# Performance work log

Hardware: AMD Instinct MI355X
Metric: run time of the kernel (lower is better)

## Reference

```python
import jax, jax.numpy as jnp
import numpy as np

BLKQ = 64
BLKK = 64
TOPK_RATIO = 0.125  # ratio of key blocks kept per query block


def setup_inputs() -> dict:
    key = jax.random.key(0)
    k0, k1, k2, k3 = jax.random.split(key, 4)
    B, H, L, D = 2, 16, 2048, 128
    q = jax.random.normal(k0, (B, H, L, D), dtype=jnp.float32)
    k = jax.random.normal(k1, (B, H, L, D), dtype=jnp.float32)
    v = jax.random.normal(k2, (B, H, L, D), dtype=jnp.float32)
    # proj_l is zero-init in the module; use small random weights so the branch is exercised
    w_proj = jax.random.normal(k3, (D, D), dtype=jnp.float32) * 0.02
    b_proj = jnp.zeros((D,), dtype=jnp.float32)
    return {"q": q, "k": k, "v": v, "w_proj": w_proj, "b_proj": b_proj}


def _forward(q, k, v, w_proj, b_proj):
    B, H, L, D = q.shape
    nQ, nK = L // BLKQ, L // BLKK
    real_topk = max(1, int(TOPK_RATIO * nK))
    scale = 1.0 / jnp.sqrt(jnp.float32(D))

    # ---- block map (get_block_map): mean-pooled block scores -> top-k key blocks per query block ----
    qb = q.reshape(B, H, nQ, BLKQ, D).mean(axis=3)            # (B,H,nQ,D)
    kb = k.reshape(B, H, nK, BLKK, D).mean(axis=3)            # (B,H,nK,D)
    blk_scores = jnp.einsum('bhqd,bhkd->bhqk', qb, kb)        # (B,H,nQ,nK)
    _, lut = jax.lax.top_k(jax.lax.stop_gradient(blk_scores), real_topk)  # (B,H,nQ,T) int32

    # ---- block-sparse softmax attention over the selected key blocks ----
    kblk = k.reshape(B, H, nK, BLKK, D)
    vblk = v.reshape(B, H, nK, BLKK, D)
    idx = lut[:, :, :, :, None, None]                         # (B,H,nQ,T,1,1)
    kg = jnp.take_along_axis(kblk[:, :, None], idx, axis=3)   # (B,H,nQ,T,BLKK,D)
    vg = jnp.take_along_axis(vblk[:, :, None], idx, axis=3)   # (B,H,nQ,T,BLKK,D)
    T = real_topk
    kg = kg.reshape(B, H, nQ, T * BLKK, D)
    vg = vg.reshape(B, H, nQ, T * BLKK, D)
    qr = q.reshape(B, H, nQ, BLKQ, D)
    s = jnp.einsum('bhqid,bhqjd->bhqij', qr, kg) * scale      # (B,H,nQ,BLKQ,T*BLKK)
    p = jax.nn.softmax(s, axis=-1)
    o_s = jnp.einsum('bhqij,bhqjd->bhqid', p, vg).reshape(B, H, L, D)

    # ---- linear (kernelized) attention branch, feature_map = softmax over D ----
    phi_q = jax.nn.softmax(q, axis=-1)
    phi_k = jax.nn.softmax(k, axis=-1)
    kvsum = jnp.einsum('bhld,bhle->bhde', phi_k, v)           # (B,H,D,D)
    ksum = phi_k.sum(axis=2)                                  # (B,H,D)
    num = jnp.einsum('bhld,bhde->bhle', phi_q, kvsum)         # (B,H,L,D)
    den = 1e-5 + jnp.einsum('bhld,bhd->bhl', phi_q, ksum)[..., None]
    o_l = num / den
    o_l = o_l @ w_proj.T + b_proj                             # nn.Linear

    return o_s + o_l                                          # (B,H,L,D)


def reference(q, k, v, w_proj, b_proj):
    return _forward(q, k, v, w_proj, b_proj)
```

## Files before the change

### kernel.cpp

```cpp
#include <hip/hip_runtime.h>
#include <math.h>

static constexpr int BH   = 32;
static constexpr int L    = 2048;
static constexpr int D    = 128;
static constexpr int NB   = 32;
static constexpr int TOPK = 4;

static constexpr size_t QB_OFF    = 0;
static constexpr size_t KB_OFF    = 131072;
static constexpr size_t LUT_OFF   = 262144;
static constexpr size_t KS_OFF    = 266240;
static constexpr size_t A_OFF     = 270336;
static constexpr size_t PART_OFF  = 794624;
static constexpr size_t KHI_OFF   = 9183232;
static constexpr size_t KLO_OFF   = 13377536;
static constexpr size_t VTHI_OFF  = 17571840;
static constexpr size_t VTLO_OFF  = 21766144;
static constexpr size_t PHITH_OFF = 25960448;
static constexpr size_t PHITL_OFF = 30154752;

typedef __attribute__((ext_vector_type(8))) short short8;
typedef __attribute__((ext_vector_type(4))) float f32x4;

__device__ __forceinline__ unsigned short f2bf(float x) {
  unsigned u = __float_as_uint(x);
  u += 0x7fffu + ((u >> 16) & 1u);
  return (unsigned short)(u >> 16);
}
__device__ __forceinline__ float bf2f(unsigned short h) {
  return __uint_as_float(((unsigned)h) << 16);
}
__device__ __forceinline__ f32x4 mfma16(short8 a, short8 b, f32x4 c) {
  return __builtin_amdgcn_mfma_f32_16x16x32_bf16(a, b, c, 0, 0, 0);
}
__device__ __forceinline__ void gl_lds16(const void* g, void* l) {
  __builtin_amdgcn_global_load_lds(
      (const __attribute__((address_space(1))) unsigned int*)g,
      (__attribute__((address_space(3))) unsigned int*)l, 16, 0, 0);
}

__global__ __launch_bounds__(256) void k_prep(
    const float* __restrict__ q, const float* __restrict__ k, const float* __restrict__ v,
    float* __restrict__ qb, float* __restrict__ kb,
    unsigned short* __restrict__ khi, unsigned short* __restrict__ klo,
    unsigned short* __restrict__ vthi, unsigned short* __restrict__ vtlo,
    unsigned short* __restrict__ phith, unsigned short* __restrict__ phitl,
    float* __restrict__ ksum) {
  extern __shared__ float smp[];
  float* Vs   = smp;
  float* Ps   = smp + 8192;
  float* part = smp + 16384;
  int bid = blockIdx.x;
  int t = threadIdx.x;
  size_t rb = (size_t)bid * 64 * D;
  int c = t & 31, g = t >> 5;
  const float4* v4 = (const float4*)(v + rb);
  float4* Vs4 = (float4*)Vs;
  float4* Ps4 = (float4*)Ps;
#pragma unroll
  for (int it = 0; it < 8; ++it) {
    int p = t + 256 * it;
    int row = p >> 5, cq = p & 31;
    Vs4[row * 32 + (cq ^ ((row >> 2) & 7))] = v4[p];
  }
  float4 qs = {0.f, 0.f, 0.f, 0.f};
#pragma unroll
  for (int it = 0; it < 8; ++it) {
    int row = g + 8 * it;
    float4 xv = *(const float4*)(q + rb + (size_t)row * D + 4 * c);
    qs.x += xv.x; qs.y += xv.y; qs.z += xv.z; qs.w += xv.w;
  }
  ((float4*)part)[g * 32 + c] = qs;
  __syncthreads();
  if (t < 128) {
    float s = 0.f;
#pragma unroll
    for (int gg = 0; gg < 8; ++gg) s += part[gg * 128 + t];
    qb[(size_t)bid * D + t] = s * (1.f / 64.f);
  }
  __syncthreads();
  float4 ks = {0.f, 0.f, 0.f, 0.f};
#pragma unroll
  for (int it = 0; it < 8; ++it) {
    int row = g + 8 * it;
    size_t off = rb + (size_t)row * D + 4 * c;
    float4 xv = *(const float4*)(k + off);
    ushort4 h, l;
    h.x = f2bf(xv.x); l.x = f2bf(xv.x - bf2f(h.x));
    h.y = f2bf(xv.y); l.y = f2bf(xv.y - bf2f(h.y));
    h.z = f2bf(xv.z); l.z = f2bf(xv.z - bf2f(h.z));
    h.w = f2bf(xv.w); l.w = f2bf(xv.w - bf2f(h.w));
    *(ushort4*)(khi + off) = h;
    *(ushort4*)(klo + off) = l;
    ks.x += xv.x; ks.y += xv.y; ks.z += xv.z; ks.w += xv.w;
    float mx = fmaxf(fmaxf(xv.x, xv.y), fmaxf(xv.z, xv.w));
    mx = fmaxf(mx, __shfl_xor(mx, 1));
    mx = fmaxf(mx, __shfl_xor(mx, 2));
    mx = fmaxf(mx, __shfl_xor(mx, 4));
    mx = fmaxf(mx, __shfl_xor(mx, 8));
    mx = fmaxf(mx, __shfl_xor(mx, 16));
    float e0 = __expf(xv.x - mx), e1 = __expf(xv.y - mx);
    float e2 = __expf(xv.z - mx), e3 = __expf(xv.w - mx);
    float es = e0 + e1 + e2 + e3;
    es += __shfl_xor(es, 1);
    es += __shfl_xor(es, 2);
    es += __shfl_xor(es, 4);
    es += __shfl_xor(es, 8);
    es += __shfl_xor(es, 16);
    float inv = 1.f / es;
    Ps4[row * 32 + (c ^ ((row >> 2) & 7))] =
        make_float4(e0 * inv, e1 * inv, e2 * inv, e3 * inv);
  }
  ((float4*)part)[g * 32 + c] = ks;
  __syncthreads();
  if (t < 128) {
    float s = 0.f;
#pragma unroll
    for (int gg = 0; gg < 8; ++gg) s += part[gg * 128 + t];
    kb[(size_t)bid * D + t] = s * (1.f / 64.f);
  }
  __syncthreads();
  size_t tb = (size_t)bid * 8192;
#pragma unroll
  for (int pp = 0; pp < 4; ++pp) {
    int d = 32 * pp + (t >> 3);
    int jc = t & 7;
    unsigned hs[8], ls[8], phs[8], pls[8];
#pragma unroll
    for (int i = 0; i < 8; ++i) {
      int j = jc * 8 + i;
      int idx = j * 128 + (d ^ (j & 28));
      float x = Vs[idx];
      unsigned short hh = f2bf(x);
      hs[i] = hh; ls[i] = f2bf(x - bf2f(hh));
      float px = Ps[idx];
      unsigned short phh = f2bf(px);
      phs[i] = phh; pls[i] = f2bf(px - bf2f(phh));
    }
    int4 hw, lw, pw, qw;
    hw.x = (int)(hs[0] | (hs[1] << 16)); hw.y = (int)(hs[2] | (hs[3] << 16));
    hw.z = (int)(hs[4] | (hs[5] << 16)); hw.w = (int)(hs[6] | (hs[7] << 16));
    lw.x = (int)(ls[0] | (ls[1] << 16)); lw.y = (int)(ls[2] | (ls[3] << 16));
    lw.z = (int)(ls[4] | (ls[5] << 16)); lw.w = (int)(ls[6] | (ls[7] << 16));
    pw.x = (int)(phs[0] | (phs[1] << 16)); pw.y = (int)(phs[2] | (phs[3] << 16));
    pw.z = (int)(phs[4] | (phs[5] << 16)); pw.w = (int)(phs[6] | (phs[7] << 16));
    qw.x = (int)(pls[0] | (pls[1] << 16)); qw.y = (int)(pls[2] | (pls[3] << 16));
    qw.z = (int)(pls[4] | (pls[5] << 16)); qw.w = (int)(pls[6] | (pls[7] << 16));
    *(int4*)(vthi  + tb + (size_t)d * 64 + jc * 8) = hw;
    *(int4*)(vtlo  + tb + (size_t)d * 64 + jc * 8) = lw;
    *(int4*)(phith + tb + (size_t)d * 64 + jc * 8) = pw;
    *(int4*)(phitl + tb + (size_t)d * 64 + jc * 8) = qw;
  }
  if (t < 128) {
    float s = 0.f;
#pragma unroll
    for (int row = 0; row < 64; ++row) s += Ps[row * 128 + (t ^ (row & 28))];
    atomicAdd(&ksum[(size_t)(bid >> 5) * D + t], s);
  }
}

__global__ __launch_bounds__(256) void k_scores_topk(
    const float* __restrict__ qb, const float* __restrict__ kb, int* __restrict__ lut) {
  __shared__ float qs[NB * D];
  __shared__ float ks[NB * 132];
  __shared__ float sc[NB * 33];
  int bh = blockIdx.x, t = threadIdx.x;
  const float4* qg = (const float4*)(qb + (size_t)bh * NB * D);
  const float4* kg = (const float4*)(kb + (size_t)bh * NB * D);
  float4* qs4 = (float4*)qs;
  float4* ks4 = (float4*)ks;
#pragma unroll
  for (int it = 0; it < 4; ++it) {
    int p = t + 256 * it;
    int row = p >> 5, c = p & 31;
    qs4[p] = qg[p];
    ks4[row * 33 + c] = kg[p];
  }
  __syncthreads();
#pragma unroll
  for (int ss = 0; ss < 4; ++ss) {
    int idx = t + 256 * ss;
    int qr = idx >> 5, kc = idx & 31;
    float acc = 0.f;
#pragma unroll
    for (int c = 0; c < 32; ++c) {
      float4 a = qs4[qr * 32 + c];
      float4 b = ks4[kc * 33 + c];
      acc += a.x * b.x + a.y * b.y + a.z * b.z + a.w * b.w;
    }
    sc[qr * 33 + kc] = acc;
  }
  __syncthreads();
  if (t < NB) {
    unsigned mask = 0;
    for (int s = 0; s < TOPK; ++s) {
      float best = -INFINITY; int bi = 0;
      for (int j = 0; j < NB; ++j) {
        float vv = sc[t * 33 + j];
        if (!((mask >> j) & 1u) && vv > best) { best = vv; bi = j; }
      }
      mask |= 1u << bi;
      lut[((size_t)(bh * NB) + t) * TOPK + s] = bi;
    }
  }
}

__global__ __launch_bounds__(256) void k_attn(
    const float* __restrict__ q,
    const unsigned short* __restrict__ khi, const unsigned short* __restrict__ klo,
    const unsigned short* __restrict__ vthi, const unsigned short* __restrict__ vtlo,
    const int* __restrict__ lut, float* __restrict__ out) {
  extern __shared__ char sm[];
  char* KsH = sm;
  char* KsL = sm + 16384;
  char* VsH = sm + 32768;
  char* VsL = sm + 49152;
  int f = blockIdx.x;
  int n = ((f & 7) << 7) | (f >> 3);
  int qblk = n & 31, bh = n >> 5;
  int t = threadIdx.x, lane = t & 63, w = t >> 6;
  char* PwH = sm + 65536 + w * 4096;
  char* PwL = PwH + 2048;
  int lr = lane & 15, lg = lane >> 4;
  const float scale = 0.088388347648318447f;

  short8 qh[4], ql[4];
  const float* qrow = q + ((size_t)bh * L + (size_t)qblk * 64 + 16 * w + lr) * D;
#pragma unroll
  for (int s = 0; s < 4; ++s) {
    float4 x0 = *(const float4*)(qrow + 32 * s + 8 * lg);
    float4 x1 = *(const float4*)(qrow + 32 * s + 8 * lg + 4);
    float xs[8] = {x0.x, x0.y, x0.z, x0.w, x1.x, x1.y, x1.z, x1.w};
    short8 hv, lv;
#pragma unroll
    for (int i = 0; i < 8; ++i) {
      unsigned short h = f2bf(xs[i]);
      hv[i] = (short)h;
      lv[i] = (short)f2bf(xs[i] - bf2f(h));
    }
    qh[s] = hv; ql[s] = lv;
  }

  f32x4 oacc[8];
#pragma unroll
  for (int i = 0; i < 8; ++i) oacc[i] = (f32x4){0.f, 0.f, 0.f, 0.f};
  float mrun = -INFINITY, lrun = 0.f;

  const int* lp = lut + ((size_t)bh * NB + qblk) * TOPK;
  for (int itb = 0; itb < TOPK; ++itb) {
    int kblk = lp[itb];
    __syncthreads();
    {
      const char* kbh = (const char*)(khi + ((size_t)bh * L + (size_t)kblk * 64) * D);
      const char* kbl = (const char*)(klo + ((size_t)bh * L + (size_t)kblk * 64) * D);
      const char* vbh = (const char*)(vthi + ((size_t)(bh * NB + kblk)) * 8192);
      const char* vbl = (const char*)(vtlo + ((size_t)(bh * NB + kblk)) * 8192);
#pragma unroll
      for (int jj = 0; jj < 4; ++jj) {
        int ib = 4 * w + jj;
        {
          int lrow = 4 * ib + (lane >> 4);
          int soff = lrow * 256 + (((lane & 15) ^ (lrow & 7)) << 4);
          gl_lds16(kbh + soff, KsH + ib * 1024);
          gl_lds16(kbl + soff, KsL + ib * 1024);
        }
        {
          int lrow = 8 * ib + (lane >> 3);
          int soff = lrow * 128 + (((lane & 7) ^ (lrow & 7)) << 4);
          gl_lds16(vbh + soff, VsH + ib * 1024);
          gl_lds16(vbl + soff, VsL + ib * 1024);
        }
      }
    }
    __syncthreads();
    f32x4 sacc[4];
#pragma unroll
    for (int i = 0; i < 4; ++i) sacc[i] = (f32x4){0.f, 0.f, 0.f, 0.f};
#pragma unroll
    for (int s = 0; s < 4; ++s) {
#pragma unroll
      for (int tk = 0; tk < 4; ++tk) {
        int krow = 16 * tk + lr;
        int off = krow * 256 + (((4 * s + lg) ^ (krow & 7)) << 4);
        short8 kH = *(const short8*)(KsH + off);
        short8 kL = *(const short8*)(KsL + off);
        sacc[tk] = mfma16(kH, qh[s], sacc[tk]);
        sacc[tk] = mfma16(kL, qh[s], sacc[tk]);
        sacc[tk] = mfma16(kH, ql[s], sacc[tk]);
      }
    }
    float mloc = -INFINITY;
#pragma unroll
    for (int tk = 0; tk < 4; ++tk)
#pragma unroll
      for (int r = 0; r < 4; ++r) mloc = fmaxf(mloc, sacc[tk][r]);
    mloc = fmaxf(mloc, __shfl_xor(mloc, 16));
    mloc = fmaxf(mloc, __shfl_xor(mloc, 32));
    float mnew = fmaxf(mrun, mloc * scale);
    float alpha = __expf(mrun - mnew);
    float lloc = 0.f;
#pragma unroll
    for (int tk = 0; tk < 4; ++tk) {
      unsigned ph[4], pl[4];
#pragma unroll
      for (int r = 0; r < 4; ++r) {
        float pf = __expf(sacc[tk][r] * scale - mnew);
        lloc += pf;
        unsigned short hh = f2bf(pf);
        ph[r] = hh; pl[r] = f2bf(pf - bf2f(hh));
      }
      int j0b = 32 * tk + 8 * lg;
      int slot16 = j0b >> 4, half = (j0b >> 3) & 1;
      int off = lr * 128 + ((slot16 ^ (lr & 7)) << 4) + half * 8;
      *(int2*)(PwH + off) = make_int2((int)(ph[0] | (ph[1] << 16)),
                                      (int)(ph[2] | (ph[3] << 16)));
      *(int2*)(PwL + off) = make_int2((int)(pl[0] | (pl[1] << 16)),
                                      (int)(pl[2] | (pl[3] << 16)));
    }
    lloc += __shfl_xor(lloc, 16);
    lloc += __shfl_xor(lloc, 32);
    lrun = lrun * alpha + lloc;
    mrun = mnew;
    float ar[4];
#pragma unroll
    for (int r = 0; r < 4; ++r) ar[r] = __shfl(alpha, 4 * lg + r);
#pragma unroll
    for (int tv = 0; tv < 8; ++tv)
#pragma unroll
      for (int r = 0; r < 4; ++r) oacc[tv][r] *= ar[r];
#pragma unroll
    for (int ks = 0; ks < 2; ++ks) {
      int poff = lr * 128 + (((lg + 4 * ks) ^ (lr & 7)) << 4);
      short8 pH = *(const short8*)(PwH + poff);
      short8 pL = *(const short8*)(PwL + poff);
#pragma unroll
      for (int tv = 0; tv < 8; ++tv) {
        int vrow = 16 * tv + lr;
        int voff = vrow * 128 + (((lg + 4 * ks) ^ (vrow & 7)) << 4);
        short8 vH = *(const short8*)(VsH + voff);
        short8 vL = *(const short8*)(VsL + voff);
        oacc[tv] = mfma16(pH, vH, oacc[tv]);
        oacc[tv] = mfma16(pL, vH, oacc[tv]);
        oacc[tv] = mfma16(pH, vL, oacc[tv]);
      }
    }
  }
  float rinv[4];
#pragma unroll
  for (int r = 0; r < 4; ++r) rinv[r] = 1.f / __shfl(lrun, 4 * lg + r);
  float* ob = out + ((size_t)bh * L + (size_t)qblk * 64 + 16 * w) * D;
#pragma unroll
  for (int tv = 0; tv < 8; ++tv)
#pragma unroll
    for (int r = 0; r < 4; ++r)
      ob[(size_t)(4 * lg + r) * D + 16 * tv + lr] = oacc[tv][r] * rinv[r];
}

__global__ __launch_bounds__(256) void k_kvmm(
    const unsigned short* __restrict__ vthi, const unsigned short* __restrict__ vtlo,
    const unsigned short* __restrict__ phith, const unsigned short* __restrict__ phitl,
    float* __restrict__ part) {
  int slice = blockIdx.x, bh = blockIdx.y;
  int t = threadIdx.x, lane = t & 63, w = t >> 6;
  int lr = lane & 15, lg = lane >> 4;
  f32x4 acc[2][8];
#pragma unroll
  for (int et = 0; et < 2; ++et)
#pragma unroll
    for (int dt = 0; dt < 8; ++dt) acc[et][dt] = (f32x4){0.f, 0.f, 0.f, 0.f};
#pragma unroll
  for (int ks = 0; ks < 4; ++ks) {
    int kblk = 2 * slice + (ks >> 1);
    int li = 32 * (ks & 1);
    size_t base = ((size_t)(bh * NB + kblk)) * 8192 + li + 8 * lg;
    short8 aH[2], aL[2];
#pragma unroll
    for (int et = 0; et < 2; ++et) {
      int e = 32 * w + 16 * et + lr;
      aH[et] = *(const short8*)(vthi + base + (size_t)e * 64);
      aL[et] = *(const short8*)(vtlo + base + (size_t)e * 64);
    }
#pragma unroll
    for (int dt = 0; dt < 8; ++dt) {
      int d = 16 * dt + lr;
      short8 bH = *(const short8*)(phith + base + (size_t)d * 64);
      short8 bL = *(const short8*)(phitl + base + (size_t)d * 64);
#pragma unroll
      for (int et = 0; et < 2; ++et) {
        acc[et][dt] = mfma16(aH[et], bH, acc[et][dt]);
        acc[et][dt] = mfma16(aL[et], bH, acc[et][dt]);
        acc[et][dt] = mfma16(aH[et], bL, acc[et][dt]);
      }
    }
  }
  float* pb = part + ((size_t)(bh * 16 + slice)) * 16384;
#pragma unroll
  for (int et = 0; et < 2; ++et)
#pragma unroll
    for (int dt = 0; dt < 8; ++dt)
#pragma unroll
      for (int r = 0; r < 4; ++r)
        pb[(size_t)(32 * w + 16 * et + 4 * lg + r) * 128 + 16 * dt + lr] =
            acc[et][dt][r];
}

__global__ __launch_bounds__(256) void k_projA(
    const float* __restrict__ part, const float* __restrict__ w, float* __restrict__ A) {
  extern __shared__ float smA[];
  float* wts   = smA;
  float* kvred = smA + 16384;
  int dquad = blockIdx.x, bh = blockIdx.y;
  int t = threadIdx.x;
  const float4* wg = (const float4*)w;
#pragma unroll
  for (int it = 0; it < 16; ++it) {
    int p4 = t + 256 * it;
    int j = p4 >> 5, ebase = (p4 & 31) << 2;
    float4 val = wg[p4];
    wts[(ebase + 0) * D + ((j + ebase + 0) & 127)] = val.x;
    wts[(ebase + 1) * D + ((j + ebase + 1) & 127)] = val.y;
    wts[(ebase + 2) * D + ((j + ebase + 2) & 127)] = val.z;
    wts[(ebase + 3) * D + ((j + ebase + 3) & 127)] = val.w;
  }
#pragma unroll
  for (int u = 0; u < 4; ++u) {
    int f4id = t + 256 * u;
    int e = f4id >> 3, dl4 = f4id & 7;
    float4 acc4 = {0.f, 0.f, 0.f, 0.f};
#pragma unroll
    for (int s = 0; s < 16; ++s) {
      float4 p = *(const float4*)(part + ((size_t)(bh * 16 + s)) * 16384 +
                                  (size_t)e * 128 + dquad * 32 + dl4 * 4);
      acc4.x += p.x; acc4.y += p.y; acc4.z += p.z; acc4.w += p.w;
    }
    *(float4*)(kvred + e * 32 + dl4 * 4) = acc4;
  }
  __syncthreads();
  int j = t & 127, dh = t >> 7;
  int dbase = dquad * 32 + dh * 16;
  float acc[16];
#pragma unroll
  for (int u = 0; u < 16; ++u) acc[u] = 0.f;
  for (int e = 0; e < D; ++e) {
    float wv = wts[e * D + ((j + e) & 127)];
#pragma unroll
    for (int dd = 0; dd < 16; ++dd)
      acc[dd] += kvred[e * 32 + dh * 16 + dd] * wv;
  }
#pragma unroll
  for (int dd = 0; dd < 16; ++dd)
    A[((size_t)(bh * D + dbase + dd)) * D + j] = acc[dd];
}

__global__ __launch_bounds__(256) void k_linear_out(
    const float* __restrict__ q, const float* __restrict__ A,
    const float* __restrict__ ksum, const float* __restrict__ bproj,
    float* __restrict__ out) {
  extern __shared__ float smf[];
  float* As    = smf;
  float* phis  = smf + 16384;
  float* ksums = smf + 16384 + 32 * 132;
  int rb = blockIdx.x, bh = blockIdx.y;
  int t = threadIdx.x;
  int r = t >> 3, sub = t & 7;
  const float4* Ag = (const float4*)(A + (size_t)bh * D * D);
  float4* As4 = (float4*)As;
#pragma unroll
  for (int it = 0; it < 16; ++it) {
    int p = t + 256 * it;
    As4[p] = Ag[p];
  }
  if (t < D) ksums[t] = ksum[bh * D + t];
  int row = rb * 32 + r;
  const float4* qr4 = (const float4*)(q + ((size_t)(bh * L + row)) * D) + sub * 4;
  float x[16];
  {
    float4 a0 = qr4[0], a1 = qr4[1], a2 = qr4[2], a3 = qr4[3];
    x[0]=a0.x; x[1]=a0.y; x[2]=a0.z; x[3]=a0.w;
    x[4]=a1.x; x[5]=a1.y; x[6]=a1.z; x[7]=a1.w;
    x[8]=a2.x; x[9]=a2.y; x[10]=a2.z; x[11]=a2.w;
    x[12]=a3.x; x[13]=a3.y; x[14]=a3.z; x[15]=a3.w;
  }
  float mx = -INFINITY;
#pragma unroll
  for (int u = 0; u < 16; ++u) mx = fmaxf(mx, x[u]);
  mx = fmaxf(mx, __shfl_xor(mx, 1));
  mx = fmaxf(mx, __shfl_xor(mx, 2));
  mx = fmaxf(mx, __shfl_xor(mx, 4));
  float es = 0.f;
#pragma unroll
  for (int u = 0; u < 16; ++u) { x[u] = __expf(x[u] - mx); es += x[u]; }
  es += __shfl_xor(es, 1);
  es += __shfl_xor(es, 2);
  es += __shfl_xor(es, 4);
  float inv = 1.f / es;
  __syncthreads();
  float dloc = 0.f;
#pragma unroll
  for (int u = 0; u < 16; ++u) {
    float ph = x[u] * inv;
    phis[r * 132 + sub * 16 + u] = ph;
    dloc += ph * ksums[sub * 16 + u];
  }
  dloc += __shfl_xor(dloc, 1);
  dloc += __shfl_xor(dloc, 2);
  dloc += __shfl_xor(dloc, 4);
  float rden = 1.f / (1e-5f + dloc);
  __syncthreads();
  float4 acc[4];
#pragma unroll
  for (int ee = 0; ee < 4; ++ee) { acc[ee].x = 0.f; acc[ee].y = 0.f; acc[ee].z = 0.f; acc[ee].w = 0.f; }
  for (int f = 0; f < D; ++f) {
    float ph = phis[r * 132 + f];
#pragma unroll
    for (int ee = 0; ee < 4; ++ee) {
      float4 av = As4[f * 32 + sub + (ee << 3)];
      acc[ee].x += ph * av.x;
      acc[ee].y += ph * av.y;
      acc[ee].z += ph * av.z;
      acc[ee].w += ph * av.w;
    }
  }
  float4* og = (float4*)(out + ((size_t)(bh * L + row)) * D);
  const float4* bg = (const float4*)bproj;
#pragma unroll
  for (int ee = 0; ee < 4; ++ee) {
    int c = sub + (ee << 3);
    float4 oo = og[c];
    float4 bb = bg[c];
    oo.x += acc[ee].x * rden + bb.x;
    oo.y += acc[ee].y * rden + bb.y;
    oo.z += acc[ee].z * rden + bb.z;
    oo.w += acc[ee].w * rden + bb.w;
    og[c] = oo;
  }
}

extern "C" void kernel_launch(void* const* d_in, const int* in_sizes, int n_in,
                              void* d_out, int out_size, void* d_ws, size_t ws_size,
                              hipStream_t stream) {
  const float* q = (const float*)d_in[0];
  const float* k = (const float*)d_in[1];
  const float* v = (const float*)d_in[2];
  const float* w = (const float*)d_in[3];
  const float* b = (const float*)d_in[4];
  float* out = (float*)d_out;
  float* ws = (float*)d_ws;
  float* qb    = ws + QB_OFF;
  float* kb    = ws + KB_OFF;
  int*   lut   = (int*)(ws + LUT_OFF);
  float* ksum  = ws + KS_OFF;
  float* A     = ws + A_OFF;
  float* partb = ws + PART_OFF;
  unsigned short* khi   = (unsigned short*)(ws + KHI_OFF);
  unsigned short* klo   = (unsigned short*)(ws + KLO_OFF);
  unsigned short* vthi  = (unsigned short*)(ws + VTHI_OFF);
  unsigned short* vtlo  = (unsigned short*)(ws + VTLO_OFF);
  unsigned short* phith = (unsigned short*)(ws + PHITH_OFF);
  unsigned short* phitl = (unsigned short*)(ws + PHITL_OFF);

  hipFuncSetAttribute(reinterpret_cast<const void*>(k_prep),
                      hipFuncAttributeMaxDynamicSharedMemorySize, 69632);
  hipFuncSetAttribute(reinterpret_cast<const void*>(k_attn),
                      hipFuncAttributeMaxDynamicSharedMemorySize, 81920);
  hipFuncSetAttribute(reinterpret_cast<const void*>(k_projA),
                      hipFuncAttributeMaxDynamicSharedMemorySize, 81920);
  hipFuncSetAttribute(reinterpret_cast<const void*>(k_linear_out),
                      hipFuncAttributeMaxDynamicSharedMemorySize, 82944);

  hipMemsetAsync(ksum, 0, 4096 * sizeof(float), stream);

  k_prep       <<<dim3(BH * NB), dim3(256), 69632, stream>>>(
      q, k, v, qb, kb, khi, klo, vthi, vtlo, phith, phitl, ksum);
  k_scores_topk<<<dim3(BH),      dim3(256), 0, stream>>>(qb, kb, lut);
  k_attn       <<<dim3(NB * BH), dim3(256), 81920, stream>>>(
      q, khi, klo, vthi, vtlo, lut, out);
  k_kvmm       <<<dim3(16, BH),  dim3(256), 0, stream>>>(
      vthi, vtlo, phith, phitl, partb);
  k_projA      <<<dim3(4, BH),   dim3(256), 81920, stream>>>(partb, w, A);
  k_linear_out <<<dim3(64, BH),  dim3(256), 82944, stream>>>(q, A, ksum, b, out);
}
```

Before: 331.2 us.

## Run linear-attention output GEMM on MFMA with split-bf16 transposed A

k_projA now writes the projected KV matrix transposed, as high and low bf16 halves. A new k_linout kernel replaces the scalar FP32 LDS-based k_linear_out: it computes phi(q) in registers, splits it into bf16 hi/lo, and runs the 64x128x128 product with three MFMA passes per tile, reading A directly from global memory. The aim is to replace scalar FMA work and the 80KB shared-memory staging with matrix cores and to use fewer, larger blocks. Precision relies on the three-term bf16 split, and A is now read from global or cache per wave.

```diff
diff --git a/kernel.cpp b/kernel.cpp
--- a/kernel.cpp
+++ b/kernel.cpp
@@ -11,7 +11,8 @@
 static constexpr size_t KB_OFF    = 131072;
 static constexpr size_t LUT_OFF   = 262144;
 static constexpr size_t KS_OFF    = 266240;
-static constexpr size_t A_OFF     = 270336;
+static constexpr size_t ATHI_OFF  = 270336;
+static constexpr size_t ATLO_OFF  = 532480;
 static constexpr size_t PART_OFF  = 794624;
 static constexpr size_t KHI_OFF   = 9183232;
 static constexpr size_t KLO_OFF   = 13377536;
@@ -406,7 +407,8 @@
 }
 
 __global__ __launch_bounds__(256) void k_projA(
-    const float* __restrict__ part, const float* __restrict__ w, float* __restrict__ A) {
+    const float* __restrict__ part, const float* __restrict__ w,
+    unsigned short* __restrict__ athi, unsigned short* __restrict__ atlo) {
   extern __shared__ float smA[];
   float* wts   = smA;
   float* kvred = smA + 16384;
@@ -448,92 +450,107 @@
     for (int dd = 0; dd < 16; ++dd)
       acc[dd] += kvred[e * 32 + dh * 16 + dd] * wv;
   }
-#pragma unroll
-  for (int dd = 0; dd < 16; ++dd)
-    A[((size_t)(bh * D + dbase + dd)) * D + j] = acc[dd];
-}
-
-__global__ __launch_bounds__(256) void k_linear_out(
-    const float* __restrict__ q, const float* __restrict__ A,
-    const float* __restrict__ ksum, const float* __restrict__ bproj,
-    float* __restrict__ out) {
-  extern __shared__ float smf[];
-  float* As    = smf;
-  float* phis  = smf + 16384;
-  float* ksums = smf + 16384 + 32 * 132;
-  int rb = blockIdx.x, bh = blockIdx.y;
-  int t = threadIdx.x;
-  int r = t >> 3, sub = t & 7;
-  const float4* Ag = (const float4*)(A + (size_t)bh * D * D);
-  float4* As4 = (float4*)As;
-#pragma unroll
-  for (int it = 0; it < 16; ++it) {
-    int p = t + 256 * it;
-    As4[p] = Ag[p];
-  }
-  if (t < D) ksums[t] = ksum[bh * D + t];
-  int row = rb * 32 + r;
-  const float4* qr4 = (const float4*)(q + ((size_t)(bh * L + row)) * D) + sub * 4;
-  float x[16];
-  {
-    float4 a0 = qr4[0], a1 = qr4[1], a2 = qr4[2], a3 = qr4[3];
-    x[0]=a0.x; x[1]=a0.y; x[2]=a0.z; x[3]=a0.w;
-    x[4]=a1.x; x[5]=a1.y; x[6]=a1.z; x[7]=a1.w;
-    x[8]=a2.x; x[9]=a2.y; x[10]=a2.z; x[11]=a2.w;
-    x[12]=a3.x; x[13]=a3.y; x[14]=a3.z; x[15]=a3.w;
-  }
+  unsigned hs[16], ls[16];
+#pragma unroll
+  for (int dd = 0; dd < 16; ++dd) {
+    unsigned short hh = f2bf(acc[dd]);
+    hs[dd] = hh; ls[dd] = f2bf(acc[dd] - bf2f(hh));
+  }
+  size_t ab = ((size_t)bh * D + j) * D + dbase;
+  int4 h0, h1, l0, l1;
+  h0.x = (int)(hs[0] | (hs[1] << 16));   h0.y = (int)(hs[2] | (hs[3] << 16));
+  h0.z = (int)(hs[4] | (hs[5] << 16));   h0.w = (int)(hs[6] | (hs[7] << 16));
+  h1.x = (int)(hs[8] | (hs[9] << 16));   h1.y = (int)(hs[10] | (hs[11] << 16));
+  h1.z = (int)(hs[12] | (hs[13] << 16)); h1.w = (int)(hs[14] | (hs[15] << 16));
+  l0.x = (int)(ls[0] | (ls[1] << 16));   l0.y = (int)(ls[2] | (ls[3] << 16));
+  l0.z = (int)(ls[4] | (ls[5] << 16));   l0.w = (int)(ls[6] | (ls[7] << 16));
+  l1.x = (int)(ls[8] | (ls[9] << 16));   l1.y = (int)(ls[10] | (ls[11] << 16));
+  l1.z = (int)(ls[12] | (ls[13] << 16)); l1.w = (int)(ls[14] | (ls[15] << 16));
+  *(int4*)(athi + ab) = h0;  *(int4*)(athi + ab + 8) = h1;
+  *(int4*)(atlo + ab) = l0;  *(int4*)(atlo + ab + 8) = l1;
+}
+
+__global__ __launch_bounds__(256) void k_linout(
+    const float* __restrict__ q, const unsigned short* __restrict__ athi,
+    const unsigned short* __restrict__ atlo, const float* __restrict__ ksum,
+    const float* __restrict__ bproj, float* __restrict__ out) {
+  int qblk = blockIdx.x, bh = blockIdx.y;
+  int t = threadIdx.x, lane = t & 63, w = t >> 6;
+  int lr = lane & 15, lg = lane >> 4;
+  const float* qrow = q + ((size_t)bh * L + (size_t)qblk * 64 + 16 * w + lr) * D;
+  float xs[4][8];
   float mx = -INFINITY;
 #pragma unroll
-  for (int u = 0; u < 16; ++u) mx = fmaxf(mx, x[u]);
-  mx = fmaxf(mx, __shfl_xor(mx, 1));
-  mx = fmaxf(mx, __shfl_xor(mx, 2));
-  mx = fmaxf(mx, __shfl_xor(mx, 4));
+  for (int s = 0; s < 4; ++s) {
+    float4 x0 = *(const float4*)(qrow + 32 * s + 8 * lg);
+    float4 x1 = *(const float4*)(qrow + 32 * s + 8 * lg + 4);
+    xs[s][0] = x0.x; xs[s][1] = x0.y; xs[s][2] = x0.z; xs[s][3] = x0.w;
+    xs[s][4] = x1.x; xs[s][5] = x1.y; xs[s][6] = x1.z; xs[s][7] = x1.w;
+#pragma unroll
+    for (int i = 0; i < 8; ++i) mx = fmaxf(mx, xs[s][i]);
+  }
+  mx = fmaxf(mx, __shfl_xor(mx, 16));
+  mx = fmaxf(mx, __shfl_xor(mx, 32));
   float es = 0.f;
 #pragma unroll
-  for (int u = 0; u < 16; ++u) { x[u] = __expf(x[u] - mx); es += x[u]; }
-  es += __shfl_xor(es, 1);
-  es += __shfl_xor(es, 2);
-  es += __shfl_xor(es, 4);
+  for (int s = 0; s < 4; ++s)
+#pragma unroll
+    for (int i = 0; i < 8; ++i) { xs[s][i] = __expf(xs[s][i] - mx); es += xs[s][i]; }
+  es += __shfl_xor(es, 16);
+  es += __shfl_xor(es, 32);
   float inv = 1.f / es;
-  __syncthreads();
-  float dloc = 0.f;
-#pragma unroll
-  for (int u = 0; u < 16; ++u) {
-    float ph = x[u] * inv;
-    phis[r * 132 + sub * 16 + u] = ph;
-    dloc += ph * ksums[sub * 16 + u];
-  }
-  dloc += __shfl_xor(dloc, 1);
-  dloc += __shfl_xor(dloc, 2);
-  dloc += __shfl_xor(dloc, 4);
-  float rden = 1.f / (1e-5f + dloc);
-  __syncthreads();
-  float4 acc[4];
-#pragma unroll
-  for (int ee = 0; ee < 4; ++ee) { acc[ee].x = 0.f; acc[ee].y = 0.f; acc[ee].z = 0.f; acc[ee].w = 0.f; }
-  for (int f = 0; f < D; ++f) {
-    float ph = phis[r * 132 + f];
-#pragma unroll
-    for (int ee = 0; ee < 4; ++ee) {
-      float4 av = As4[f * 32 + sub + (ee << 3)];
-      acc[ee].x += ph * av.x;
-      acc[ee].y += ph * av.y;
-      acc[ee].z += ph * av.z;
-      acc[ee].w += ph * av.w;
-    }
-  }
-  float4* og = (float4*)(out + ((size_t)(bh * L + row)) * D);
+  const float* kp = ksum + (size_t)bh * D;
+  float dpart = 0.f;
+  short8 phH[4], phL[4];
+#pragma unroll
+  for (int s = 0; s < 4; ++s) {
+    float4 k0 = *(const float4*)(kp + 32 * s + 8 * lg);
+    float4 k1 = *(const float4*)(kp + 32 * s + 8 * lg + 4);
+    float kk[8] = {k0.x, k0.y, k0.z, k0.w, k1.x, k1.y, k1.z, k1.w};
+    short8 hv, lv;
+#pragma unroll
+    for (int i = 0; i < 8; ++i) {
+      float p = xs[s][i] * inv;
+      dpart += p * kk[i];
+      unsigned short hh = f2bf(p);
+      hv[i] = (short)hh;
+      lv[i] = (short)f2bf(p - bf2f(hh));
+    }
+    phH[s] = hv; phL[s] = lv;
+  }
+  dpart += __shfl_xor(dpart, 16);
+  dpart += __shfl_xor(dpart, 32);
+  float rden = 1.f / (1e-5f + dpart);
+  f32x4 acc[8];
+#pragma unroll
+  for (int dt = 0; dt < 8; ++dt) acc[dt] = (f32x4){0.f, 0.f, 0.f, 0.f};
+  const unsigned short* ah = athi + (size_t)bh * D * D;
+  const unsigned short* al = atlo + (size_t)bh * D * D;
+#pragma unroll
+  for (int s = 0; s < 4; ++s) {
+#pragma unroll
+    for (int dt = 0; dt < 8; ++dt) {
+      size_t off = (size_t)(16 * dt + lr) * D + 32 * s + 8 * lg;
+      short8 aH = *(const short8*)(ah + off);
+      short8 aL = *(const short8*)(al + off);
+      acc[dt] = mfma16(aH, phH[s], acc[dt]);
+      acc[dt] = mfma16(aL, phH[s], acc[dt]);
+      acc[dt] = mfma16(aH, phL[s], acc[dt]);
+    }
+  }
+  float* ob = out + ((size_t)bh * L + (size_t)qblk * 64 + 16 * w + lr) * D;
+  float4* og4 = (float4*)ob;
   const float4* bg = (const float4*)bproj;
 #pragma unroll
-  for (int ee = 0; ee < 4; ++ee) {
-    int c = sub + (ee << 3);
-    float4 oo = og[c];
-    float4 bb = bg[c];
-    oo.x += acc[ee].x * rden + bb.x;
-    oo.y += acc[ee].y * rden + bb.y;
-    oo.z += acc[ee].z * rden + bb.z;
-    oo.w += acc[ee].w * rden + bb.w;
-    og[c] = oo;
+  for (int dt = 0; dt < 8; ++dt) {
+    int c4 = 4 * dt + lg;
+    float4 oo = og4[c4];
+    float4 bb = bg[c4];
+    oo.x += acc[dt][0] * rden + bb.x;
+    oo.y += acc[dt][1] * rden + bb.y;
+    oo.z += acc[dt][2] * rden + bb.z;
+    oo.w += acc[dt][3] * rden + bb.w;
+    og4[c4] = oo;
   }
 }
 
@@ -551,8 +568,9 @@
   float* kb    = ws + KB_OFF;
   int*   lut   = (int*)(ws + LUT_OFF);
   float* ksum  = ws + KS_OFF;
-  float* A     = ws + A_OFF;
   float* partb = ws + PART_OFF;
+  unsigned short* athi  = (unsigned short*)(ws + ATHI_OFF);
+  unsigned short* atlo  = (unsigned short*)(ws + ATLO_OFF);
   unsigned short* khi   = (unsigned short*)(ws + KHI_OFF);
   unsigned short* klo   = (unsigned short*)(ws + KLO_OFF);
   unsigned short* vthi  = (unsigned short*)(ws + VTHI_OFF);
@@ -566,8 +584,6 @@
                       hipFuncAttributeMaxDynamicSharedMemorySize, 81920);
   hipFuncSetAttribute(reinterpret_cast<const void*>(k_projA),
                       hipFuncAttributeMaxDynamicSharedMemorySize, 81920);
-  hipFuncSetAttribute(reinterpret_cast<const void*>(k_linear_out),
-                      hipFuncAttributeMaxDynamicSharedMemorySize, 82944);
 
   hipMemsetAsync(ksum, 0, 4096 * sizeof(float), stream);
 
@@ -578,6 +594,6 @@
       q, khi, klo, vthi, vtlo, lut, out);
   k_kvmm       <<<dim3(16, BH),  dim3(256), 0, stream>>>(
       vthi, vtlo, phith, phitl, partb);
-  k_projA      <<<dim3(4, BH),   dim3(256), 81920, stream>>>(partb, w, A);
-  k_linear_out <<<dim3(64, BH),  dim3(256), 82944, stream>>>(q, A, ksum, b, out);
-}
+  k_projA      <<<dim3(4, BH),   dim3(256), 81920, stream>>>(partb, w, athi, atlo);
+  k_linout     <<<dim3(NB, BH),  dim3(256), 0, stream>>>(q, athi, atlo, ksum, b, out);
+}
```

After: 299.3 us. -9.6%, faster.
